# Performance work log

Hardware: AMD Instinct MI355X
Metric: run time of the kernel (lower is better)

Reference implementation:

```python
import jax, jax.numpy as jnp
import numpy as np

NUM_ITERATIONS = 3  # dynamic routing iterations
EPS = 1e-8
IN_LEN = 8   # capsule length after conv (out_length of CapsuleConv2d)
OUT_LEN = 16
OUT_CAPS = 10


def squash(s, axis=-1):
    # v = (|s|^2 / (1+|s|^2)) * s/|s|
    n2 = jnp.sum(s * s, axis=axis, keepdims=True)
    return (n2 / (1.0 + n2)) * s * jax.lax.rsqrt(n2 + EPS)


def setup_inputs() -> dict:
    key = jax.random.key(0)
    k1, k2, k3 = jax.random.split(key, 3)
    B = 16384
    x = jax.random.normal(k1, (B, 1, 3, 3), dtype=jnp.float32)
    # CapsuleConv2d weight: standard conv kernel [out_ch, in_ch, k, k]
    conv_w = 0.1 * jax.random.normal(k2, (32, 1, 3, 3), dtype=jnp.float32)
    # CapsuleLinear routing weight: [out_capsules, in_capsules, out_length, in_length]
    lin_w = 0.1 * jax.random.normal(k3, (OUT_CAPS, 36, OUT_LEN, IN_LEN), dtype=jnp.float32)
    return {"x": x, "conv_w": conv_w, "lin_w": lin_w}


def reference(x, conv_w, lin_w):
    B = x.shape[0]
    # --- CapsuleConv2d: conv2d (stride 1, pad 1) + squash over capsule length ---
    y = jax.lax.conv_general_dilated(
        x, conv_w, window_strides=(1, 1), padding=((1, 1), (1, 1)),
        dimension_numbers=("NCHW", "OIHW", "NCHW"))  # [B,32,3,3]
    H, W = y.shape[2], y.shape[3]
    G = y.shape[1] // IN_LEN  # 4 capsule groups of 8 channels
    y = y.reshape(B, G, IN_LEN, H, W)
    y = squash(y, axis=2)
    # capsules per spatial location: [B, H*W*G, in_length] = [B,36,8]
    caps = y.transpose(0, 3, 4, 1, 2).reshape(B, H * W * G, IN_LEN)

    # --- CapsuleLinear: priors + dynamic routing by agreement ---
    # priors[b,o,i,d] = sum_l lin_w[o,i,d,l] * caps[b,i,l]
    priors = jnp.einsum("oidl,bil->boid", lin_w, caps)  # [B,10,36,16]
    logits = jnp.zeros(priors.shape[:3] + (1,), dtype=priors.dtype)  # [B,10,36,1]
    out = None
    for it in range(NUM_ITERATIONS):
        probs = jax.nn.softmax(logits, axis=1)            # coupling over out_capsules
        out = squash(jnp.sum(probs * priors, axis=2))      # [B,10,16]
        if it != NUM_ITERATIONS - 1:
            # agreement: priors . out
            logits = logits + jnp.sum(priors * out[:, :, None, :], axis=-1, keepdims=True)
    return out  # [B,10,16]
```

## Files before the change

kernel.cpp:

```cpp
#include <hip/hip_runtime.h>


constexpr int OC = 10, NI = 36, OD = 16, IL = 8;
constexpr int M  = 4;
constexpr int NT = 64 * OC;

template<int CTRL>
__device__ __forceinline__ float dpp_movf(float v) {
    return __int_as_float(__builtin_amdgcn_update_dpp(
        0, __float_as_int(v), CTRL, 0xF, 0xF, true));
}
__device__ __forceinline__ float rowsum16(float v) {
    v += dpp_movf<0xB1>(v);
    v += dpp_movf<0x4E>(v);
    v += dpp_movf<0x141>(v);
    v += dpp_movf<0x140>(v);
    return v;
}

__global__ __launch_bounds__(NT, 5)
void capsnet_kernel(const float* __restrict__ xg,
                    const float* __restrict__ cwg,
                    const float* __restrict__ lwg,
                    float* __restrict__ outg)
{
    __shared__ float xs[M * 9];
    __shared__ float cw[288];
    __shared__ float caps[M * NI * IL];
    __shared__ float pl[M * OC * NI];
    __shared__ float dl[M * OC * NI];

    const int t  = threadIdx.x;
    const int b0 = blockIdx.x * M;

    if (t < M * 9) xs[t] = xg[b0 * 9 + t];
    if (t < 288)   cw[t] = cwg[t];
    __syncthreads();

    if (t < M * NI) {
        const int m  = t / NI;
        const int ci = t % NI;
        const int cg = ci & 3;
        const int wx = (ci >> 2) % 3;
        const int hx = ci / 12;
        float acc[IL] = {};
        #pragma unroll
        for (int kh = 0; kh < 3; ++kh) {
            const int xh = hx + kh - 1;
            if (xh < 0 || xh > 2) continue;
            #pragma unroll
            for (int kw = 0; kw < 3; ++kw) {
                const int xw = wx + kw - 1;
                if (xw < 0 || xw > 2) continue;
                const float xv = xs[m * 9 + xh * 3 + xw];
                #pragma unroll
                for (int l = 0; l < IL; ++l)
                    acc[l] += xv * cw[(cg * 8 + l) * 9 + kh * 3 + kw];
            }
        }
        float n2 = 0.f;
        #pragma unroll
        for (int l = 0; l < IL; ++l) n2 += acc[l] * acc[l];
        const float sc = n2 / (1.f + n2) * rsqrtf(n2 + 1e-8f);
        #pragma unroll
        for (int l = 0; l < IL; ++l) caps[t * IL + l] = acc[l] * sc;
    }
    __syncthreads();

    const int o    = t >> 6;
    const int lane = t & 63;
    const int ig   = lane >> 4;
    const int d    = lane & 15;

    float P[M][9];
    const float* wp = lwg + ((o * NI + ig) * OD + d) * IL;

#define PRI_M(k_, m_) { \
    const float4 ca = *reinterpret_cast<const float4*>(&caps[((m_) * NI + 4*(k_) + ig) * IL]); \
    const float4 cz = *reinterpret_cast<const float4*>(&caps[((m_) * NI + 4*(k_) + ig) * IL + 4]); \
    P[m_][k_] = wa.x * ca.x + wa.y * ca.y + wa.z * ca.z + wa.w * ca.w \
              + wb.x * cz.x + wb.y * cz.y + wb.z * cz.z + wb.w * cz.w; }
#define PRI_K(k_) { \
    const float4 wa = *reinterpret_cast<const float4*>(wp + (k_) * (4 * OD * IL)); \
    const float4 wb = *reinterpret_cast<const float4*>(wp + (k_) * (4 * OD * IL) + 4); \
    PRI_M(k_, 0) PRI_M(k_, 1) PRI_M(k_, 2) PRI_M(k_, 3) }
    PRI_K(0) PRI_K(1) PRI_K(2) PRI_K(3) PRI_K(4) PRI_K(5) PRI_K(6) PRI_K(7) PRI_K(8)
#undef PRI_K
#undef PRI_M

    float ov[M];

#define IT0_M(m_) { \
    float s = P[m_][0] + P[m_][1] + P[m_][2] + P[m_][3] + P[m_][4] \
            + P[m_][5] + P[m_][6] + P[m_][7] + P[m_][8]; \
    s *= 0.1f; \
    s += __shfl_xor(s, 16); \
    s += __shfl_xor(s, 32); \
    const float n2 = rowsum16(s * s); \
    const float sc = n2 / (1.f + n2) * rsqrtf(n2 + 1e-8f); \
    ov[m_] = s * sc; }
    IT0_M(0) IT0_M(1) IT0_M(2) IT0_M(3)
#undef IT0_M

#define AG_KM(m_, k_, DST) { \
    const float a = rowsum16(P[m_][k_] * ov[m_]); \
    if (d == 0) DST[((m_) * OC + o) * NI + 4*(k_) + ig] = __expf(a); }
#define AG_M(m_, DST) \
    AG_KM(m_, 0, DST) AG_KM(m_, 1, DST) AG_KM(m_, 2, DST) AG_KM(m_, 3, DST) \
    AG_KM(m_, 4, DST) AG_KM(m_, 5, DST) AG_KM(m_, 6, DST) AG_KM(m_, 7, DST) AG_KM(m_, 8, DST)
    AG_M(0, pl) AG_M(1, pl) AG_M(2, pl) AG_M(3, pl)
    __syncthreads();

    if (t < M * NI) {
        float* base = &pl[(t / NI) * (OC * NI) + (t % NI)];
        float v[OC];
        float ss = 0.f;
#define LD1(oo) { v[oo] = base[(oo) * NI]; ss += v[oo]; }
        LD1(0) LD1(1) LD1(2) LD1(3) LD1(4) LD1(5) LD1(6) LD1(7) LD1(8) LD1(9)
#undef LD1
        const float inv = 1.f / ss;
#define ST1(oo) base[(oo) * NI] = v[oo] * inv;
        ST1(0) ST1(1) ST1(2) ST1(3) ST1(4) ST1(5) ST1(6) ST1(7) ST1(8) ST1(9)
#undef ST1
    }
    __syncthreads();

#define IT1_M(m_) { \
    const float* pb = &pl[((m_) * OC + o) * NI + ig]; \
    float s = pb[ 0] * P[m_][0] + pb[ 4] * P[m_][1] + pb[ 8] * P[m_][2] \
            + pb[12] * P[m_][3] + pb[16] * P[m_][4] + pb[20] * P[m_][5] \
            + pb[24] * P[m_][6] + pb[28] * P[m_][7] + pb[32] * P[m_][8]; \
    s += __shfl_xor(s, 16); \
    s += __shfl_xor(s, 32); \
    const float n2 = rowsum16(s * s); \
    const float sc = n2 / (1.f + n2) * rsqrtf(n2 + 1e-8f); \
    ov[m_] = s * sc; }
    IT1_M(0) IT1_M(1) IT1_M(2) IT1_M(3)

    AG_M(0, dl) AG_M(1, dl) AG_M(2, dl) AG_M(3, dl)
#undef AG_M
#undef AG_KM
    __syncthreads();

    if (t < M * NI) {
        const int off = (t / NI) * (OC * NI) + (t % NI);
        float* pb = &pl[off];
        const float* db = &dl[off];
        float v[OC];
        float ss = 0.f;
#define LD2(oo) { v[oo] = pb[(oo) * NI] * db[(oo) * NI]; ss += v[oo]; }
        LD2(0) LD2(1) LD2(2) LD2(3) LD2(4) LD2(5) LD2(6) LD2(7) LD2(8) LD2(9)
#undef LD2
        const float inv = 1.f / ss;
#define ST2(oo) pb[(oo) * NI] = v[oo] * inv;
        ST2(0) ST2(1) ST2(2) ST2(3) ST2(4) ST2(5) ST2(6) ST2(7) ST2(8) ST2(9)
#undef ST2
    }
    __syncthreads();

#define IT2_M(m_) { \
    const float* pb = &pl[((m_) * OC + o) * NI + ig]; \
    float s = pb[ 0] * P[m_][0] + pb[ 4] * P[m_][1] + pb[ 8] * P[m_][2] \
            + pb[12] * P[m_][3] + pb[16] * P[m_][4] + pb[20] * P[m_][5] \
            + pb[24] * P[m_][6] + pb[28] * P[m_][7] + pb[32] * P[m_][8]; \
    s += __shfl_xor(s, 16); \
    s += __shfl_xor(s, 32); \
    const float n2 = rowsum16(s * s); \
    const float sc = n2 / (1.f + n2) * rsqrtf(n2 + 1e-8f); \
    if (ig == 0) outg[(b0 + (m_)) * (OC * OD) + o * OD + d] = s * sc; }
    IT2_M(0) IT2_M(1) IT2_M(2) IT2_M(3)
#undef IT2_M
#undef IT1_M
}

extern "C" void kernel_launch(void* const* d_in, const int* in_sizes, int n_in,
                              void* d_out, int out_size, void* d_ws, size_t ws_size,
                              hipStream_t stream) {
    const float* x  = (const float*)d_in[0];
    const float* cwp = (const float*)d_in[1];
    const float* lw = (const float*)d_in[2];
    float* out = (float*)d_out;
    const int B = in_sizes[0] / 9;
    dim3 grid(B / M), block(NT);
    capsnet_kernel<<<grid, block, 0, stream>>>(x, cwp, lw, out);
}
```

Measured before the change: 255.0 us.

## Pad routing logit layout, vectorize LDS stores, share caps halves via DPP

Routing logits are moved to a padded per-(o,ig) row layout of 12 floats, so each writer lane stores 9 logits with two float4 stores plus a scalar, and readers fetch them with vector loads. The exp is deferred from the 360 writer lanes to the 144 normalizing threads. Each lane now loads only half of a capsule from LDS and gets the other half from its neighbour via a DPP row_ror:8, halving the caps LDS traffic per prior. The cost is strided scalar access in the normalization pass and extra DPP instructions.

```diff
diff --git a/kernel.cpp b/kernel.cpp
--- a/kernel.cpp
+++ b/kernel.cpp
@@ -4,6 +4,7 @@
 constexpr int OC = 10, NI = 36, OD = 16, IL = 8;
 constexpr int M  = 4;
 constexpr int NT = 64 * OC;
+constexpr int PROW = 12;
 
 template<int CTRL>
 __device__ __forceinline__ float dpp_movf(float v) {
@@ -27,8 +28,8 @@
     __shared__ float xs[M * 9];
     __shared__ float cw[288];
     __shared__ float caps[M * NI * IL];
-    __shared__ float pl[M * OC * NI];
-    __shared__ float dl[M * OC * NI];
+    __shared__ float pl[M * OC * 4 * PROW];
+    __shared__ float dl[M * OC * 4 * PROW];
 
     const int t  = threadIdx.x;
     const int b0 = blockIdx.x * M;
@@ -71,18 +72,25 @@
     const int lane = t & 63;
     const int ig   = lane >> 4;
     const int d    = lane & 15;
+    const int q    = d >> 3;
 
     float P[M][9];
     const float* wp = lwg + ((o * NI + ig) * OD + d) * IL;
+    const int qo = q * 4, qx = (q ^ 1) * 4;
 
 #define PRI_M(k_, m_) { \
-    const float4 ca = *reinterpret_cast<const float4*>(&caps[((m_) * NI + 4*(k_) + ig) * IL]); \
-    const float4 cz = *reinterpret_cast<const float4*>(&caps[((m_) * NI + 4*(k_) + ig) * IL + 4]); \
-    P[m_][k_] = wa.x * ca.x + wa.y * ca.y + wa.z * ca.z + wa.w * ca.w \
-              + wb.x * cz.x + wb.y * cz.y + wb.z * cz.z + wb.w * cz.w; }
+    const float4 co = *reinterpret_cast<const float4*>( \
+        &caps[((m_) * NI + 4*(k_) + ig) * IL + qo]); \
+    float4 cx; \
+    cx.x = dpp_movf<0x128>(co.x); \
+    cx.y = dpp_movf<0x128>(co.y); \
+    cx.z = dpp_movf<0x128>(co.z); \
+    cx.w = dpp_movf<0x128>(co.w); \
+    P[m_][k_] = wq.x * co.x + wq.y * co.y + wq.z * co.z + wq.w * co.w \
+              + wr.x * cx.x + wr.y * cx.y + wr.z * cx.z + wr.w * cx.w; }
 #define PRI_K(k_) { \
-    const float4 wa = *reinterpret_cast<const float4*>(wp + (k_) * (4 * OD * IL)); \
-    const float4 wb = *reinterpret_cast<const float4*>(wp + (k_) * (4 * OD * IL) + 4); \
+    const float4 wq = *reinterpret_cast<const float4*>(wp + (k_) * (4 * OD * IL) + qo); \
+    const float4 wr = *reinterpret_cast<const float4*>(wp + (k_) * (4 * OD * IL) + qx); \
     PRI_M(k_, 0) PRI_M(k_, 1) PRI_M(k_, 2) PRI_M(k_, 3) }
     PRI_K(0) PRI_K(1) PRI_K(2) PRI_K(3) PRI_K(4) PRI_K(5) PRI_K(6) PRI_K(7) PRI_K(8)
 #undef PRI_K
@@ -102,34 +110,48 @@
     IT0_M(0) IT0_M(1) IT0_M(2) IT0_M(3)
 #undef IT0_M
 
-#define AG_KM(m_, k_, DST) { \
-    const float a = rowsum16(P[m_][k_] * ov[m_]); \
-    if (d == 0) DST[((m_) * OC + o) * NI + 4*(k_) + ig] = __expf(a); }
-#define AG_M(m_, DST) \
-    AG_KM(m_, 0, DST) AG_KM(m_, 1, DST) AG_KM(m_, 2, DST) AG_KM(m_, 3, DST) \
-    AG_KM(m_, 4, DST) AG_KM(m_, 5, DST) AG_KM(m_, 6, DST) AG_KM(m_, 7, DST) AG_KM(m_, 8, DST)
+#define AG_M(m_, DST) { \
+    const float a0 = rowsum16(P[m_][0] * ov[m_]); \
+    const float a1 = rowsum16(P[m_][1] * ov[m_]); \
+    const float a2 = rowsum16(P[m_][2] * ov[m_]); \
+    const float a3 = rowsum16(P[m_][3] * ov[m_]); \
+    const float a4 = rowsum16(P[m_][4] * ov[m_]); \
+    const float a5 = rowsum16(P[m_][5] * ov[m_]); \
+    const float a6 = rowsum16(P[m_][6] * ov[m_]); \
+    const float a7 = rowsum16(P[m_][7] * ov[m_]); \
+    const float a8 = rowsum16(P[m_][8] * ov[m_]); \
+    if (d == 0) { \
+        float* wb = &DST[(((m_) * OC + o) * 4 + ig) * PROW]; \
+        *reinterpret_cast<float4*>(wb)     = make_float4(a0, a1, a2, a3); \
+        *reinterpret_cast<float4*>(wb + 4) = make_float4(a4, a5, a6, a7); \
+        wb[8] = a8; \
+    } }
     AG_M(0, pl) AG_M(1, pl) AG_M(2, pl) AG_M(3, pl)
     __syncthreads();
 
     if (t < M * NI) {
-        float* base = &pl[(t / NI) * (OC * NI) + (t % NI)];
+        const int m = t / NI, r = t % NI;
+        float* base = &pl[(m * OC * 4 + (r / 9)) * PROW + (r % 9)];
         float v[OC];
         float ss = 0.f;
-#define LD1(oo) { v[oo] = base[(oo) * NI]; ss += v[oo]; }
+#define LD1(oo) { v[oo] = __expf(base[(oo) * 4 * PROW]); ss += v[oo]; }
         LD1(0) LD1(1) LD1(2) LD1(3) LD1(4) LD1(5) LD1(6) LD1(7) LD1(8) LD1(9)
 #undef LD1
         const float inv = 1.f / ss;
-#define ST1(oo) base[(oo) * NI] = v[oo] * inv;
+#define ST1(oo) base[(oo) * 4 * PROW] = v[oo] * inv;
         ST1(0) ST1(1) ST1(2) ST1(3) ST1(4) ST1(5) ST1(6) ST1(7) ST1(8) ST1(9)
 #undef ST1
     }
     __syncthreads();
 
 #define IT1_M(m_) { \
-    const float* pb = &pl[((m_) * OC + o) * NI + ig]; \
-    float s = pb[ 0] * P[m_][0] + pb[ 4] * P[m_][1] + pb[ 8] * P[m_][2] \
-            + pb[12] * P[m_][3] + pb[16] * P[m_][4] + pb[20] * P[m_][5] \
-            + pb[24] * P[m_][6] + pb[28] * P[m_][7] + pb[32] * P[m_][8]; \
+    const float* pb = &pl[(((m_) * OC + o) * 4 + ig) * PROW]; \
+    const float4 pA = *reinterpret_cast<const float4*>(pb); \
+    const float4 pB = *reinterpret_cast<const float4*>(pb + 4); \
+    const float p8  = pb[8]; \
+    float s = pA.x * P[m_][0] + pA.y * P[m_][1] + pA.z * P[m_][2] + pA.w * P[m_][3] \
+            + pB.x * P[m_][4] + pB.y * P[m_][5] + pB.z * P[m_][6] + pB.w * P[m_][7] \
+            + p8   * P[m_][8]; \
     s += __shfl_xor(s, 16); \
     s += __shfl_xor(s, 32); \
     const float n2 = rowsum16(s * s); \
@@ -139,30 +161,33 @@
 
     AG_M(0, dl) AG_M(1, dl) AG_M(2, dl) AG_M(3, dl)
 #undef AG_M
-#undef AG_KM
     __syncthreads();
 
     if (t < M * NI) {
-        const int off = (t / NI) * (OC * NI) + (t % NI);
+        const int m = t / NI, r = t % NI;
+        const int off = (m * OC * 4 + (r / 9)) * PROW + (r % 9);
         float* pb = &pl[off];
         const float* db = &dl[off];
         float v[OC];
         float ss = 0.f;
-#define LD2(oo) { v[oo] = pb[(oo) * NI] * db[(oo) * NI]; ss += v[oo]; }
+#define LD2(oo) { v[oo] = pb[(oo) * 4 * PROW] * __expf(db[(oo) * 4 * PROW]); ss += v[oo]; }
         LD2(0) LD2(1) LD2(2) LD2(3) LD2(4) LD2(5) LD2(6) LD2(7) LD2(8) LD2(9)
 #undef LD2
         const float inv = 1.f / ss;
-#define ST2(oo) pb[(oo) * NI] = v[oo] * inv;
+#define ST2(oo) pb[(oo) * 4 * PROW] = v[oo] * inv;
         ST2(0) ST2(1) ST2(2) ST2(3) ST2(4) ST2(5) ST2(6) ST2(7) ST2(8) ST2(9)
 #undef ST2
     }
     __syncthreads();
 
 #define IT2_M(m_) { \
-    const float* pb = &pl[((m_) * OC + o) * NI + ig]; \
-    float s = pb[ 0] * P[m_][0] + pb[ 4] * P[m_][1] + pb[ 8] * P[m_][2] \
-            + pb[12] * P[m_][3] + pb[16] * P[m_][4] + pb[20] * P[m_][5] \
-            + pb[24] * P[m_][6] + pb[28] * P[m_][7] + pb[32] * P[m_][8]; \
+    const float* pb = &pl[(((m_) * OC + o) * 4 + ig) * PROW]; \
+    const float4 pA = *reinterpret_cast<const float4*>(pb); \
+    const float4 pB = *reinterpret_cast<const float4*>(pb + 4); \
+    const float p8  = pb[8]; \
+    float s = pA.x * P[m_][0] + pA.y * P[m_][1] + pA.z * P[m_][2] + pA.w * P[m_][3] \
+            + pB.x * P[m_][4] + pB.y * P[m_][5] + pB.z * P[m_][6] + pB.w * P[m_][7] \
+            + p8   * P[m_][8]; \
     s += __shfl_xor(s, 16); \
     s += __shfl_xor(s, 32); \
     const float n2 = rowsum16(s * s); \
```

After: 238.2 us. 1.07x faster.
